# Kernel tuning notes

Measured on AMD Instinct MI355X. Metric: run time of the kernel, lower is better.

The kernel has to match this reference:

```python
import jax, jax.numpy as jnp
import numpy as np

L, BAT, A, B, D, NBITS = 2, 32, 64, 1024, 128, 1024
PADDING = 0


def setup_inputs() -> dict:
    key = jax.random.key(0)
    k1, k2, k3, k4, k5 = jax.random.split(key, 5)
    query_embed = jax.random.normal(k1, (L, BAT, A, D), dtype=jnp.float32)
    doc_embed = jax.random.normal(k2, (L, BAT, B, D), dtype=jnp.float32)
    query_tok = jax.random.randint(k3, (BAT, A), 0, 2)
    doc_tok = jax.random.randint(k4, (BAT, B), 0, 2)
    # LSH projection matrix: randn * sigma + mu with sigma=0.1, mu=0
    r = jax.random.normal(k5, (NBITS, D), dtype=jnp.float32) * 0.1
    return {"query_embed": query_embed, "doc_embed": doc_embed,
            "query_tok": query_tok, "doc_tok": doc_tok, "r": r}


def reference(query_embed, doc_embed, query_tok, doc_tok, r):
    d = r.shape[0]  # num_bits
    # sign-hash: (emb @ r.T > 0).float()  -> binary codes in {0,1}
    c1 = (jnp.einsum('lbad,kd->lbak', query_embed, r) > 0).astype(jnp.float32)  # [L,BAT,A,NBITS]
    c2 = (jnp.einsum('lbcd,kd->lbck', doc_embed, r) > 0).astype(jnp.float32)    # [L,BAT,B,NBITS]
    # Hamming distance via popcount identity: |u-v|_H = sum(u) + sum(v) - 2 u.v
    s1 = c1.sum(-1)  # [L,BAT,A]
    s2 = c2.sum(-1)  # [L,BAT,B]
    dot = jnp.einsum('lbak,lbck->lbac', c1, c2)  # [L,BAT,A,B]
    ham = s1[..., :, None] + s2[..., None, :] - 2.0 * dot
    sim = jnp.cos(jnp.pi / d * ham)  # [L,BAT,A,B]
    # zero out padded query / doc positions
    qmask = (query_tok == PADDING)[None, :, :, None]
    dmask = (doc_tok == PADDING)[None, :, None, :]
    sim = jnp.where(qmask | dmask, 0.0, sim)
    # torch.stack(simmat, dim=1) -> [BAT, L, A, B]
    return jnp.transpose(sim, (1, 0, 2, 3))
```

## Files before the change

### kernel.cpp

```cpp
#include <hip/hip_runtime.h>
#include <math.h>

#define L_ 2
#define BAT_ 32
#define A_ 64
#define B_ 1024
#define D_ 128
#define NBITS_ 1024
#define NW 32
#define NQROWS (L_*BAT_*A_)
#define NDROWS (L_*BAT_*B_)
#define NROWS (NQROWS + NDROWS)

#define TM 128
#define TN 128
#define KH 32
#define RS 72

typedef __bf16 bf16x4 __attribute__((ext_vector_type(4)));
typedef __bf16 bf16x8 __attribute__((ext_vector_type(8)));
typedef float  f32x4  __attribute__((ext_vector_type(4)));

__global__ __launch_bounds__(256) void hash_kernel(
    const float* __restrict__ qe, const float* __restrict__ de,
    const float* __restrict__ r, unsigned int* __restrict__ codes_t)
{
    __shared__ __align__(16) __bf16 As[TM * RS];
    __shared__ __align__(16) __bf16 Bs[TN * RS];

    const int t = threadIdx.x;
    const int row0 = blockIdx.x * TM;
    const int bit0 = blockIdx.y * TN;

    const float* abase = (row0 < NQROWS) ? (qe + (size_t)row0 * D_)
                                         : (de + (size_t)(row0 - NQROWS) * D_);
    const float* bbase = r + (size_t)bit0 * D_;

    const int wv   = t >> 6;
    const int lane = t & 63;
    const int quad = lane >> 4;
    const int col  = lane & 15;
    const int wrow = (wv >> 1) * 64;
    const int wbit = (wv & 1) * 64;

    f32x4 acc[4][4];
    #pragma unroll
    for (int ti = 0; ti < 4; ++ti)
        #pragma unroll
        for (int tj = 0; tj < 4; ++tj)
            acc[ti][tj] = (f32x4){0.f, 0.f, 0.f, 0.f};

    #pragma unroll
    for (int ks = 0; ks < D_; ks += KH) {
        if (ks) __syncthreads();
        #pragma unroll
        for (int i = 0; i < 4; ++i) {
            int f = (t + i * 256) * 4;
            int rr = f >> 5, cc = f & 31;
            float4 v = *(const float4*)(abase + (size_t)rr * D_ + ks + cc);
            bf16x4 hi, lo;
            hi[0] = (__bf16)v.x; hi[1] = (__bf16)v.y;
            hi[2] = (__bf16)v.z; hi[3] = (__bf16)v.w;
            lo[0] = (__bf16)(v.x - (float)hi[0]);
            lo[1] = (__bf16)(v.y - (float)hi[1]);
            lo[2] = (__bf16)(v.z - (float)hi[2]);
            lo[3] = (__bf16)(v.w - (float)hi[3]);
            *(bf16x4*)(&As[rr * RS + cc])      = hi;
            *(bf16x4*)(&As[rr * RS + 32 + cc]) = lo;
        }
        #pragma unroll
        for (int i = 0; i < 4; ++i) {
            int f = (t + i * 256) * 4;
            int rr = f >> 5, cc = f & 31;
            float4 v = *(const float4*)(bbase + (size_t)rr * D_ + ks + cc);
            bf16x4 hi, lo;
            hi[0] = (__bf16)v.x; hi[1] = (__bf16)v.y;
            hi[2] = (__bf16)v.z; hi[3] = (__bf16)v.w;
            lo[0] = (__bf16)(v.x - (float)hi[0]);
            lo[1] = (__bf16)(v.y - (float)hi[1]);
            lo[2] = (__bf16)(v.z - (float)hi[2]);
            lo[3] = (__bf16)(v.w - (float)hi[3]);
            *(bf16x4*)(&Bs[rr * RS + cc])      = hi;
            *(bf16x4*)(&Bs[rr * RS + 32 + cc]) = lo;
        }
        __syncthreads();

        #pragma unroll
        for (int seg = 0; seg < 3; ++seg) {
            const int ao = (seg == 2) ? 32 : 0;
            const int bo = (seg == 1) ? 32 : 0;
            bf16x8 af[4], bfr[4];
            #pragma unroll
            for (int ti = 0; ti < 4; ++ti)
                af[ti] = *(const bf16x8*)(
                    &As[(wrow + ti * 16 + col) * RS + ao + quad * 8]);
            #pragma unroll
            for (int tj = 0; tj < 4; ++tj)
                bfr[tj] = *(const bf16x8*)(
                    &Bs[(wbit + tj * 16 + col) * RS + bo + quad * 8]);
            #pragma unroll
            for (int ti = 0; ti < 4; ++ti)
                #pragma unroll
                for (int tj = 0; tj < 4; ++tj)
                    acc[ti][tj] = __builtin_amdgcn_mfma_f32_16x16x32_bf16(
                        af[ti], bfr[tj], acc[ti][tj], 0, 0, 0);
        }
    }

    #pragma unroll
    for (int ti = 0; ti < 4; ++ti) {
        #pragma unroll
        for (int rg = 0; rg < 4; ++rg) {
            unsigned long long b[4];
            #pragma unroll
            for (int tj = 0; tj < 4; ++tj)
                b[tj] = __ballot(acc[ti][tj][rg] > 0.f);
            if (col < 2) {
                const int w = col;
                unsigned int lo16 = (unsigned int)(b[2 * w]     >> (16 * quad)) & 0xFFFFu;
                unsigned int hi16 = (unsigned int)(b[2 * w + 1] >> (16 * quad)) & 0xFFFFu;
                const int row = row0 + wrow + ti * 16 + quad * 4 + rg;
                const int wg  = blockIdx.y * 4 + (wv & 1) * 2 + w;
                codes_t[(size_t)wg * NROWS + row] = lo16 | (hi16 << 16);
            }
        }
    }
}

__global__ __launch_bounds__(256) void simmat_kernel(
    const unsigned int* __restrict__ codes_t,
    const int* __restrict__ qtok, const int* __restrict__ dtok,
    float* __restrict__ out)
{
    __shared__ unsigned int qc[8 * 36];

    const int blk  = blockIdx.x;
    const int ct   = blk & 3;
    const int asub = (blk >> 2) & 7;
    const int b    = (blk >> 5) & 31;
    const int l    = blk >> 10;
    const int t    = threadIdx.x;

    const int a0 = asub * 8;
    const int qrow0 = (l * BAT_ + b) * A_ + a0;
    if (t < 256) {
        int w = t >> 3, a = t & 7;
        qc[a * 36 + w] = codes_t[(size_t)w * NROWS + qrow0 + a];
    }
    __syncthreads();

    const int c = ct * 256 + t;
    const size_t drow = (size_t)NQROWS + (size_t)(l * BAT_ + b) * B_ + c;
    unsigned int dc[NW];
    #pragma unroll
    for (int w = 0; w < NW; ++w) dc[w] = codes_t[(size_t)w * NROWS + drow];
    const float dm = (dtok[b * B_ + c] != 0) ? 1.f : 0.f;

    float* obase = out + ((size_t)((b * L_ + l) * A_ + a0)) * B_ + c;
    #pragma unroll
    for (int ai = 0; ai < 8; ++ai) {
        int ham = 0;
        #pragma unroll
        for (int m = 0; m < 8; ++m) {
            uint4 qv = *(const uint4*)(&qc[ai * 36 + m * 4]);
            ham += __popc(qv.x ^ dc[4 * m])     + __popc(qv.y ^ dc[4 * m + 1])
                 + __popc(qv.z ^ dc[4 * m + 2]) + __popc(qv.w ^ dc[4 * m + 3]);
        }
        const float qmv = (qtok[b * A_ + a0 + ai] != 0) ? 1.f : 0.f;
        float sim = __cosf((float)M_PI / (float)NBITS_ * (float)ham);
        obase[(size_t)ai * B_] = sim * (qmv * dm);
    }
}

extern "C" void kernel_launch(void* const* d_in, const int* in_sizes, int n_in,
                              void* d_out, int out_size, void* d_ws, size_t ws_size,
                              hipStream_t stream) {
    const float* qe  = (const float*)d_in[0];
    const float* de  = (const float*)d_in[1];
    const int* qtok  = (const int*)d_in[2];
    const int* dtok  = (const int*)d_in[3];
    const float* r   = (const float*)d_in[4];
    float* out = (float*)d_out;
    unsigned int* codes_t = (unsigned int*)d_ws;

    dim3 g1(NROWS / TM, NBITS_ / TN);
    hash_kernel<<<g1, 256, 0, stream>>>(qe, de, r, codes_t);
    simmat_kernel<<<L_ * BAT_ * 8 * 4, 256, 0, stream>>>(codes_t, qtok, dtok, out);
}
```

Measured before the change: 172.3 us.

## Pre-split embeddings into swizzled bf16 hi/lo fragments consumed directly by MFMA

Adds a pre-pass kernel that converts the fp32 embeddings and projection matrix once into bf16 hi/lo pairs, stored in a layout that matches the MFMA fragment order. The hash GEMM then loads fragments straight from global memory, with no LDS staging or syncthreads. Before, every one of the eight bit-tile blocks in a row redid the conversion. The cost is an extra kernel launch, a round trip through workspace memory, and global loads in the GEMM with no LDS reuse of fragments shared across the block's waves.

Result: faster. 161.0 us (-6.6%).

```diff
diff --git a/kernel.cpp b/kernel.cpp
--- a/kernel.cpp
+++ b/kernel.cpp
@@ -11,37 +11,73 @@
 #define NQROWS (L_*BAT_*A_)
 #define NDROWS (L_*BAT_*B_)
 #define NROWS (NQROWS + NDROWS)
+#define NAGRP (NROWS / 16)
+#define NBGRP (NBITS_ / 16)
 
 #define TM 128
 #define TN 128
-#define KH 32
-#define RS 72
-
-typedef __bf16 bf16x4 __attribute__((ext_vector_type(4)));
+
 typedef __bf16 bf16x8 __attribute__((ext_vector_type(8)));
 typedef float  f32x4  __attribute__((ext_vector_type(4)));
 
+__global__ __launch_bounds__(256) void preswz_kernel(
+    const float* __restrict__ qe, const float* __restrict__ de,
+    const float* __restrict__ r, __bf16* __restrict__ asw,
+    __bf16* __restrict__ rsw)
+{
+    const int g = blockIdx.x;
+    const int t = threadIdx.x;
+    const int ks = t >> 7, kk = (t >> 6) & 1, quad = (t >> 4) & 3, col = t & 15;
+
+    const float* src;
+    __bf16* dst;
+    if (g < NAGRP) {
+        int row = g * 16 + col;
+        src = (row < NQROWS) ? (qe + (size_t)row * D_)
+                             : (de + (size_t)(row - NQROWS) * D_);
+        dst = asw + (size_t)g * 4096;
+    } else {
+        int bit = (g - NAGRP) * 16 + col;
+        src = r + (size_t)bit * D_;
+        dst = rsw + (size_t)(g - NAGRP) * 4096;
+    }
+
+    const int ko = ks * 64 + kk * 32 + quad * 8;
+    float4 v0 = *(const float4*)(src + ko);
+    float4 v1 = *(const float4*)(src + ko + 4);
+    bf16x8 hi, lo;
+    hi[0] = (__bf16)v0.x; hi[1] = (__bf16)v0.y;
+    hi[2] = (__bf16)v0.z; hi[3] = (__bf16)v0.w;
+    hi[4] = (__bf16)v1.x; hi[5] = (__bf16)v1.y;
+    hi[6] = (__bf16)v1.z; hi[7] = (__bf16)v1.w;
+    lo[0] = (__bf16)(v0.x - (float)hi[0]);
+    lo[1] = (__bf16)(v0.y - (float)hi[1]);
+    lo[2] = (__bf16)(v0.z - (float)hi[2]);
+    lo[3] = (__bf16)(v0.w - (float)hi[3]);
+    lo[4] = (__bf16)(v1.x - (float)hi[4]);
+    lo[5] = (__bf16)(v1.y - (float)hi[5]);
+    lo[6] = (__bf16)(v1.z - (float)hi[6]);
+    lo[7] = (__bf16)(v1.w - (float)hi[7]);
+
+    const int c_hi = ks * 16 + kk * 4 + quad;
+    const int c_lo = c_hi + 8;
+    *(bf16x8*)(dst + (size_t)(c_hi * 16 + col) * 8) = hi;
+    *(bf16x8*)(dst + (size_t)(c_lo * 16 + col) * 8) = lo;
+}
+
 __global__ __launch_bounds__(256) void hash_kernel(
-    const float* __restrict__ qe, const float* __restrict__ de,
-    const float* __restrict__ r, unsigned int* __restrict__ codes_t)
+    const __bf16* __restrict__ asw, const __bf16* __restrict__ rsw,
+    unsigned int* __restrict__ codes_t)
 {
-    __shared__ __align__(16) __bf16 As[TM * RS];
-    __shared__ __align__(16) __bf16 Bs[TN * RS];
-
     const int t = threadIdx.x;
-    const int row0 = blockIdx.x * TM;
-    const int bit0 = blockIdx.y * TN;
-
-    const float* abase = (row0 < NQROWS) ? (qe + (size_t)row0 * D_)
-                                         : (de + (size_t)(row0 - NQROWS) * D_);
-    const float* bbase = r + (size_t)bit0 * D_;
-
     const int wv   = t >> 6;
     const int lane = t & 63;
     const int quad = lane >> 4;
     const int col  = lane & 15;
     const int wrow = (wv >> 1) * 64;
     const int wbit = (wv & 1) * 64;
+    const int ga0 = (blockIdx.x * TM + wrow) >> 4;
+    const int gb0 = (blockIdx.y * TN + wbit) >> 4;
 
     f32x4 acc[4][4];
     #pragma unroll
@@ -51,62 +87,50 @@
             acc[ti][tj] = (f32x4){0.f, 0.f, 0.f, 0.f};
 
     #pragma unroll
-    for (int ks = 0; ks < D_; ks += KH) {
-        if (ks) __syncthreads();
-        #pragma unroll
-        for (int i = 0; i < 4; ++i) {
-            int f = (t + i * 256) * 4;
-            int rr = f >> 5, cc = f & 31;
-            float4 v = *(const float4*)(abase + (size_t)rr * D_ + ks + cc);
-            bf16x4 hi, lo;
-            hi[0] = (__bf16)v.x; hi[1] = (__bf16)v.y;
-            hi[2] = (__bf16)v.z; hi[3] = (__bf16)v.w;
-            lo[0] = (__bf16)(v.x - (float)hi[0]);
-            lo[1] = (__bf16)(v.y - (float)hi[1]);
-            lo[2] = (__bf16)(v.z - (float)hi[2]);
-            lo[3] = (__bf16)(v.w - (float)hi[3]);
-            *(bf16x4*)(&As[rr * RS + cc])      = hi;
-            *(bf16x4*)(&As[rr * RS + 32 + cc]) = lo;
-        }
-        #pragma unroll
-        for (int i = 0; i < 4; ++i) {
-            int f = (t + i * 256) * 4;
-            int rr = f >> 5, cc = f & 31;
-            float4 v = *(const float4*)(bbase + (size_t)rr * D_ + ks + cc);
-            bf16x4 hi, lo;
-            hi[0] = (__bf16)v.x; hi[1] = (__bf16)v.y;
-            hi[2] = (__bf16)v.z; hi[3] = (__bf16)v.w;
-            lo[0] = (__bf16)(v.x - (float)hi[0]);
-            lo[1] = (__bf16)(v.y - (float)hi[1]);
-            lo[2] = (__bf16)(v.z - (float)hi[2]);
-            lo[3] = (__bf16)(v.w - (float)hi[3]);
-            *(bf16x4*)(&Bs[rr * RS + cc])      = hi;
-            *(bf16x4*)(&Bs[rr * RS + 32 + cc]) = lo;
-        }
-        __syncthreads();
-
-        #pragma unroll
-        for (int seg = 0; seg < 3; ++seg) {
-            const int ao = (seg == 2) ? 32 : 0;
-            const int bo = (seg == 1) ? 32 : 0;
-            bf16x8 af[4], bfr[4];
-            #pragma unroll
-            for (int ti = 0; ti < 4; ++ti)
-                af[ti] = *(const bf16x8*)(
-                    &As[(wrow + ti * 16 + col) * RS + ao + quad * 8]);
+    for (int ks = 0; ks < 2; ++ks) {
+        #pragma unroll
+        for (int kk = 0; kk < 2; ++kk) {
+            const int cbi_h = ks * 4 + kk;
+            const int cbi_l = cbi_h + 2;
+            bf16x8 ahi[4], bhi[4], alo[4], blo[4];
+            #pragma unroll
+            for (int ti = 0; ti < 4; ++ti)
+                ahi[ti] = *(const bf16x8*)(
+                    asw + (((size_t)(ga0 + ti) * 8 + cbi_h) * 64 + lane) * 8);
             #pragma unroll
             for (int tj = 0; tj < 4; ++tj)
-                bfr[tj] = *(const bf16x8*)(
-                    &Bs[(wbit + tj * 16 + col) * RS + bo + quad * 8]);
+                bhi[tj] = *(const bf16x8*)(
+                    rsw + (((size_t)(gb0 + tj) * 8 + cbi_h) * 64 + lane) * 8);
             #pragma unroll
             for (int ti = 0; ti < 4; ++ti)
                 #pragma unroll
                 for (int tj = 0; tj < 4; ++tj)
                     acc[ti][tj] = __builtin_amdgcn_mfma_f32_16x16x32_bf16(
-                        af[ti], bfr[tj], acc[ti][tj], 0, 0, 0);
+                        ahi[ti], bhi[tj], acc[ti][tj], 0, 0, 0);
+            #pragma unroll
+            for (int ti = 0; ti < 4; ++ti)
+                alo[ti] = *(const bf16x8*)(
+                    asw + (((size_t)(ga0 + ti) * 8 + cbi_l) * 64 + lane) * 8);
+            #pragma unroll
+            for (int ti = 0; ti < 4; ++ti)
+                #pragma unroll
+                for (int tj = 0; tj < 4; ++tj)
+                    acc[ti][tj] = __builtin_amdgcn_mfma_f32_16x16x32_bf16(
+                        alo[ti], bhi[tj], acc[ti][tj], 0, 0, 0);
+            #pragma unroll
+            for (int tj = 0; tj < 4; ++tj)
+                blo[tj] = *(const bf16x8*)(
+                    rsw + (((size_t)(gb0 + tj) * 8 + cbi_l) * 64 + lane) * 8);
+            #pragma unroll
+            for (int ti = 0; ti < 4; ++ti)
+                #pragma unroll
+                for (int tj = 0; tj < 4; ++tj)
+                    acc[ti][tj] = __builtin_amdgcn_mfma_f32_16x16x32_bf16(
+                        ahi[ti], blo[tj], acc[ti][tj], 0, 0, 0);
         }
     }
 
+    const int row0 = blockIdx.x * TM;
     #pragma unroll
     for (int ti = 0; ti < 4; ++ti) {
         #pragma unroll
@@ -181,9 +205,13 @@
     const int* dtok  = (const int*)d_in[3];
     const float* r   = (const float*)d_in[4];
     float* out = (float*)d_out;
+
     unsigned int* codes_t = (unsigned int*)d_ws;
-
+    __bf16* rsw = (__bf16*)((char*)d_ws + 8912896);
+    __bf16* asw = (__bf16*)((char*)d_ws + 8912896 + 524288);
+
+    preswz_kernel<<<NAGRP + NBGRP, 256, 0, stream>>>(qe, de, r, asw, rsw);
     dim3 g1(NROWS / TM, NBITS_ / TN);
-    hash_kernel<<<g1, 256, 0, stream>>>(qe, de, r, codes_t);
+    hash_kernel<<<g1, 256, 0, stream>>>(asw, rsw, codes_t);
     simmat_kernel<<<L_ * BAT_ * 8 * 4, 256, 0, stream>>>(codes_t, qtok, dtok, out);
 }
```
